# Performance work log

Hardware: AMD Instinct MI355X
Metric: run time of the kernel (lower is better)

## Reference

```python
import jax, jax.numpy as jnp
import numpy as np

N, T, DF, H, NH, E = 512, 60, 6, 64, 2, 8192
NEG = -1e10

def _leaky(x):
    return jnp.where(x >= 0, x, 0.01 * x)

def _ln(x, g, b, eps=1e-5):
    m = x.mean(-1, keepdims=True)
    v = ((x - m) ** 2).mean(-1, keepdims=True)
    return (x - m) / jnp.sqrt(v + eps) * g + b

def _gru_layer(xs, wih, whh, bih, bhh):
    # xs: (N, T, H_in) -> (N, T, H); torch GRU gate math
    h0 = jnp.zeros((xs.shape[0], whh.shape[1]), xs.dtype)
    def step(h, xt):
        gi = xt @ wih.T + bih
        gh = h @ whh.T + bhh
        ir, iz, inn = jnp.split(gi, 3, -1)
        hr, hz, hn = jnp.split(gh, 3, -1)
        r = jax.nn.sigmoid(ir + hr)
        z = jax.nn.sigmoid(iz + hz)
        n = jnp.tanh(inn + r * hn)
        h = (1 - z) * n + z * h
        return h, h
    _, hs = jax.lax.scan(step, h0, jnp.swapaxes(xs, 0, 1))
    return jnp.swapaxes(hs, 0, 1)

def _forward(x, edge_index, fc_in_w, fc_in_b, gru_wih0, gru_whh0, gru_bih0, gru_bhh0, gru_wih1, gru_whh1, gru_bih1, gru_bhh1, dm_qw, dm_kw, dm_vw, dm_vb, ssa_qw, ssa_kw, ssa_vw, ssa_vb, ln1_g, ln1_b, ln2_g, ln2_b, mlp_w1, mlp_b1, mlp_w2, mlp_b2, mha_in_w, mha_in_b, mha_out_w, mha_out_b, gf_xs_w, gf_xt_w, gf_xt_b, gf_h_w, gf_h_b, lin_w, lin_b):
    h = x @ fc_in_w.T + fc_in_b                      # (N, T, H)
    # temporal encoder: 2-layer GRU + leaky relu
    g = _gru_layer(h, gru_wih0, gru_whh0, gru_bih0, gru_bhh0)
    g = _gru_layer(g, gru_wih1, gru_whh1, gru_bih1, gru_bhh1)
    ts = _leaky(g)
    res_ts = ts[:, -1, :]                            # (N, H)
    # spatial sparse transformer: time T acts as batch, attention over stocks N
    xs = jnp.swapaxes(h, 0, 1)                       # (T, N, H)
    hd = H // NH
    q = (xs @ dm_qw.T).reshape(T, N, NH, hd).transpose(0, 2, 1, 3)
    k = (xs @ dm_kw.T).reshape(T, N, NH, hd).transpose(0, 2, 1, 3)
    v = (xs @ dm_vw.T + dm_vb).reshape(T, N, NH, hd).transpose(0, 2, 1, 3)
    attn = jnp.einsum('thnd,thmd->thnm', q, k) * (H ** -0.5)  # scale uses full dim C, as in source
    dmask = attn >= attn.mean(-1, keepdims=True)     # dynamic per-row mean threshold
    attn_s = jax.nn.softmax(jnp.where(dmask, attn, NEG), axis=-1)
    dyn = jnp.einsum('thnm,thmd->thnd', attn_s, v).transpose(0, 2, 1, 3).reshape(T, N, H)
    # SSA: static graph mask from edge_index
    qs = xs @ ssa_qw.T
    ks2 = xs @ ssa_kw.T
    vs = xs @ ssa_vw.T + ssa_vb
    a2 = jnp.einsum('tnc,tmc->tnm', qs, ks2) * (H ** -0.5)
    adj = jnp.zeros((N, N), jnp.float32).at[edge_index[0], edge_index[1]].add(1.0)
    gmask = adj >= 1.0
    a2s = jax.nn.softmax(jnp.where(gmask[None, :, :], a2, NEG), axis=-1)
    stat = jnp.einsum('tnm,tmc->tnc', a2s, vs)
    residual = dyn + stat + xs
    o = _ln(residual, ln1_g, ln1_b)
    o = (o @ mlp_w1.T + mlp_b1) @ mlp_w2.T + mlp_b2  # two linears, no activation (as in source)
    o = _ln(o + residual, ln2_g, ln2_b)
    move = _leaky(o)                                 # (T, N, H)
    # spatial embedding aggregation: sinusoidal PE + 1-head MHA over time
    pos = jnp.arange(T, dtype=jnp.float32)[:, None]
    div = jnp.exp(jnp.arange(0, H, 2, dtype=jnp.float32) * (-np.log(10000.0) / H))
    pe = jnp.zeros((T, H), jnp.float32).at[:, 0::2].set(jnp.sin(pos * div)).at[:, 1::2].set(jnp.cos(pos * div))
    src = move + pe[:, None, :]
    mq, mk, mv = jnp.split(src @ mha_in_w.T + mha_in_b, 3, axis=-1)
    sc = jnp.einsum('tnh,snh->nts', mq, mk) * (H ** -0.5)
    mo = jnp.einsum('nts,snh->tnh', jax.nn.softmax(sc, -1), mv) @ mha_out_w.T + mha_out_b
    agg = mo[-1]                                     # (N, H)
    mu = agg.mean(-1, keepdims=True)
    var = ((agg - mu) ** 2).mean(-1, keepdims=True)
    agg = (agg - mu) / jnp.sqrt(var + 1e-5)          # param-free layer_norm
    # gated fusion
    zg = jax.nn.sigmoid(agg @ gf_xs_w.T + res_ts @ gf_xt_w.T + gf_xt_b)
    fused = _leaky((zg * agg + (1 - zg) * res_ts) @ gf_h_w.T + gf_h_b)
    out = (fused @ lin_w.T + lin_b)[:, 0]
    return out, attn_s

def setup_inputs() -> dict:
    key = jax.random.key(0)
    ks = jax.random.split(key, 40)
    def w(i, shape):
        return jax.random.normal(ks[i], shape, jnp.float32) * 0.05
    return {
        'x': jax.random.normal(ks[0], (N, T, DF), jnp.float32),
        'edge_index': jax.random.randint(ks[1], (2, E), 0, N),
        'fc_in_w': w(2, (H, DF)), 'fc_in_b': w(3, (H,)),
        'gru_wih0': w(4, (3 * H, H)), 'gru_whh0': w(5, (3 * H, H)), 'gru_bih0': w(6, (3 * H,)), 'gru_bhh0': w(7, (3 * H,)),
        'gru_wih1': w(8, (3 * H, H)), 'gru_whh1': w(9, (3 * H, H)), 'gru_bih1': w(10, (3 * H,)), 'gru_bhh1': w(11, (3 * H,)),
        'dm_qw': w(12, (H, H)), 'dm_kw': w(13, (H, H)), 'dm_vw': w(14, (H, H)), 'dm_vb': w(15, (H,)),
        'ssa_qw': w(16, (H, H)), 'ssa_kw': w(17, (H, H)), 'ssa_vw': w(18, (H, H)), 'ssa_vb': w(19, (H,)),
        'ln1_g': jnp.ones((H,), jnp.float32), 'ln1_b': jnp.zeros((H,), jnp.float32),
        'ln2_g': jnp.ones((H,), jnp.float32), 'ln2_b': jnp.zeros((H,), jnp.float32),
        'mlp_w1': w(20, (2 * H, H)), 'mlp_b1': w(21, (2 * H,)), 'mlp_w2': w(22, (H, 2 * H)), 'mlp_b2': w(23, (H,)),
        'mha_in_w': w(24, (3 * H, H)), 'mha_in_b': w(25, (3 * H,)), 'mha_out_w': w(26, (H, H)), 'mha_out_b': w(27, (H,)),
        'gf_xs_w': w(28, (H, H)), 'gf_xt_w': w(29, (H, H)), 'gf_xt_b': w(30, (H,)),
        'gf_h_w': w(31, (H, H)), 'gf_h_b': w(32, (H,)),
        'lin_w': w(33, (1, H)), 'lin_b': w(34, (1,)),
    }

def reference(x, edge_index, fc_in_w, fc_in_b, gru_wih0, gru_whh0, gru_bih0, gru_bhh0, gru_wih1, gru_whh1, gru_bih1, gru_bhh1, dm_qw, dm_kw, dm_vw, dm_vb, ssa_qw, ssa_kw, ssa_vw, ssa_vb, ln1_g, ln1_b, ln2_g, ln2_b, mlp_w1, mlp_b1, mlp_w2, mlp_b2, mha_in_w, mha_in_b, mha_out_w, mha_out_b, gf_xs_w, gf_xt_w, gf_xt_b, gf_h_w, gf_h_b, lin_w, lin_b):
    return _forward(x, edge_index, fc_in_w, fc_in_b, gru_wih0, gru_whh0, gru_bih0, gru_bhh0, gru_wih1, gru_whh1, gru_bih1, gru_bhh1, dm_qw, dm_kw, dm_vw, dm_vb, ssa_qw, ssa_kw, ssa_vw, ssa_vb, ln1_g, ln1_b, ln2_g, ln2_b, mlp_w1, mlp_b1, mlp_w2, mlp_b2, mha_in_w, mha_in_b, mha_out_w, mha_out_b, gf_xs_w, gf_xt_w, gf_xt_b, gf_h_w, gf_h_b, lin_w, lin_b)
```

## Files before the change

kernel.cpp:

```cpp
#include <hip/hip_runtime.h>
#include <hip/hip_bf16.h>

#define NN 512
#define TT 60
#define DFF 6
#define EE 8192
#define TN (TT*NN)
#define TCH 20
#define NCHK 3
#define SCALEV 0.125f
#define NEGV -1.0e10f

typedef __hip_bfloat16 bf16;
using bfrag8 = __attribute__((ext_vector_type(8))) short;
using facc4  = __attribute__((ext_vector_type(4))) float;

__device__ __forceinline__ float b2f(bf16 v){ return __bfloat162float(v); }
__device__ __forceinline__ bf16 f2b(float v){ return __float2bfloat16(v); }
__device__ __forceinline__ float lk(float x){ return x >= 0.f ? x : 0.01f*x; }
__device__ __forceinline__ float sgm(float x){ return 1.f/(1.f+__expf(-x)); }

__device__ __forceinline__ float ldf(const float* p, long i){ return p[i]; }
__device__ __forceinline__ float ldf(const bf16* p, long i){ return b2f(p[i]); }
__device__ __forceinline__ void stf(float* p, long i, float v){ p[i] = v; }
__device__ __forceinline__ void stf(bf16* p, long i, float v){ p[i] = f2b(v); }

__device__ __forceinline__ float4 ld4f(const float* p){ return *(const float4*)p; }
__device__ __forceinline__ float4 ld4f(const bf16* p){
  ushort4 u = *(const ushort4*)p;
  float4 f;
  f.x = b2f(*(const bf16*)&u.x);
  f.y = b2f(*(const bf16*)&u.y);
  f.z = b2f(*(const bf16*)&u.z);
  f.w = b2f(*(const bf16*)&u.w);
  return f;
}

__device__ __forceinline__ float wsum64(float v){
  #pragma unroll
  for (int off = 32; off; off >>= 1) v += __shfl_xor(v, off, 64);
  return v;
}
__device__ __forceinline__ float wmax64(float v){
  #pragma unroll
  for (int off = 32; off; off >>= 1) v = fmaxf(v, __shfl_xor(v, off, 64));
  return v;
}

__global__ __launch_bounds__(256) void k_pack(
  const float* __restrict__ qw, const float* __restrict__ kw,
  const float* __restrict__ qsw, const float* __restrict__ ksw,
  const float* __restrict__ vw, const float* __restrict__ vsw,
  const float* __restrict__ vb, const float* __restrict__ vsb,
  const int* __restrict__ ei, unsigned int* __restrict__ msk,
  float* __restrict__ Wall, float* __restrict__ bcV)
{
  __shared__ unsigned int lmsk[8192];
  int tid = threadIdx.x;
  if (blockIdx.x == 97) {
    for (int i = tid; i < 8192; i += 256) lmsk[i] = 0u;
    __syncthreads();
    for (int e = tid; e < EE; e += 256) {
      int u = ei[e], v = ei[EE + e];
      atomicOr(&lmsk[u*16 + (v >> 5)], 1u << (v & 31));
    }
    __syncthreads();
    for (int i = tid; i < 8192; i += 256) msk[i] = lmsk[i];
    return;
  }
  int idx = blockIdx.x*256 + tid;
  if (idx < 6*4096) {
    int which = idx >> 12, rem = idx & 4095;
    const float* s = (which==0)?qw:(which==1)?kw:(which==2)?qsw:(which==3)?ksw:(which==4)?vw:vsw;
    Wall[idx] = s[rem];
  } else if (idx < 6*4096 + 128) {
    int o = idx - 6*4096;
    bcV[o] = (o < 64) ? vb[o] : vsb[o-64];
  }
}

__global__ __launch_bounds__(256) void k_fcin(
  const float* __restrict__ x, const float* __restrict__ w, const float* __restrict__ b,
  float* __restrict__ xs, float* __restrict__ resid)
{
  long idx = (long)blockIdx.x*256 + threadIdx.x;
  int o = idx & 63;
  long r = idx >> 6;
  int t = (int)(r / NN), n = (int)(r % NN);
  const float* xr = x + ((long)n*TT + t)*DFF;
  const float* wr = w + o*DFF;
  float acc = 0.f;
  #pragma unroll
  for (int j = 0; j < DFF; ++j) acc = fmaf(xr[j], wr[j], acc);
  float h = __fadd_rn(acc, b[o]);
  xs[idx] = h;
  resid[idx] = h;
}

__global__ __launch_bounds__(256) void k_proj(
  const float* __restrict__ A, const float* __restrict__ Wall, const float* __restrict__ bcV,
  float* __restrict__ qkx, float* __restrict__ qkc, bf16* __restrict__ vvc)
{
  __shared__ float As[64][68];
  __shared__ float Bs[64][68];
  int rt = blockIdx.x, bcn = blockIdx.y;
  const float* B = Wall + bcn*4096;
  int tid = threadIdx.x;
  int tx = tid & 15, ty = tid >> 4;
  float acc[4][4] = {{0.f}};
  #pragma unroll
  for (int i = 0; i < 4; ++i) {
    int t = i*256 + tid;
    int m = t >> 4, kq = (t & 15)*4;
    float4 av = *(const float4*)&A[(long)(rt*64 + m)*64 + kq];
    As[kq+0][m] = av.x; As[kq+1][m] = av.y; As[kq+2][m] = av.z; As[kq+3][m] = av.w;
    float4 bv = *(const float4*)&B[(long)m*64 + kq];
    Bs[kq+0][m] = bv.x; Bs[kq+1][m] = bv.y; Bs[kq+2][m] = bv.z; Bs[kq+3][m] = bv.w;
  }
  __syncthreads();
  for (int kk = 0; kk < 64; ++kk) {
    float4 a4 = *(const float4*)&As[kk][ty*4];
    float4 b4 = *(const float4*)&Bs[kk][tx*4];
    acc[0][0] = fmaf(a4.x,b4.x,acc[0][0]); acc[0][1] = fmaf(a4.x,b4.y,acc[0][1]); acc[0][2] = fmaf(a4.x,b4.z,acc[0][2]); acc[0][3] = fmaf(a4.x,b4.w,acc[0][3]);
    acc[1][0] = fmaf(a4.y,b4.x,acc[1][0]); acc[1][1] = fmaf(a4.y,b4.y,acc[1][1]); acc[1][2] = fmaf(a4.y,b4.z,acc[1][2]); acc[1][3] = fmaf(a4.y,b4.w,acc[1][3]);
    acc[2][0] = fmaf(a4.z,b4.x,acc[2][0]); acc[2][1] = fmaf(a4.z,b4.y,acc[2][1]); acc[2][2] = fmaf(a4.z,b4.z,acc[2][2]); acc[2][3] = fmaf(a4.z,b4.w,acc[2][3]);
    acc[3][0] = fmaf(a4.w,b4.x,acc[3][0]); acc[3][1] = fmaf(a4.w,b4.y,acc[3][1]); acc[3][2] = fmaf(a4.w,b4.z,acc[3][2]); acc[3][3] = fmaf(a4.w,b4.w,acc[3][3]);
  }
  if (bcn < 4) {
    float* C = (bcn < 2) ? qkx : qkc;
    int cb = (bcn & 1)*64;
    #pragma unroll
    for (int i = 0; i < 4; ++i) {
      long ro = (long)(rt*64 + ty*4 + i)*128 + cb + tx*4;
      #pragma unroll
      for (int j = 0; j < 4; ++j) C[ro + j] = acc[i][j];
    }
  } else {
    int cb = (bcn - 4)*64;
    float bv[4];
    #pragma unroll
    for (int j = 0; j < 4; ++j) bv[j] = bcV[cb + tx*4 + j];
    #pragma unroll
    for (int i = 0; i < 4; ++i) {
      long ro = (long)(rt*64 + ty*4 + i)*128 + cb + tx*4;
      #pragma unroll
      for (int j = 0; j < 4; ++j) vvc[ro + j] = f2b(acc[i][j] + bv[j]);
    }
  }
}

template<typename TA, typename TC>
__global__ __launch_bounds__(256) void k_gemm(
  const TA* __restrict__ A, const float* __restrict__ B, const float* __restrict__ bias,
  TC* __restrict__ C, int KD, int NC, int gather)
{
  __shared__ float As[64][68];
  __shared__ float Bs[64][68];
  int rt = blockIdx.x, bcn = blockIdx.y;
  int tid = threadIdx.x;
  int tx = tid & 15, ty = tid >> 4;
  float acc[4][4] = {{0.f}};
  int nch = KD >> 6;
  for (int kc = 0; kc < nch; ++kc) {
    __syncthreads();
    #pragma unroll
    for (int i = 0; i < 4; ++i) {
      int t = i*256 + tid;
      int m = t >> 4, kq = (t & 15)*4;
      long aoff;
      int r = rt*64 + m;
      if (gather) { int n2 = r / TT, t2 = r - n2*TT; aoff = ((long)t2*NN + n2)*64 + kc*64 + kq; }
      else aoff = (long)r*KD + kc*64 + kq;
      float4 av = ld4f(A + aoff);
      As[kq+0][m] = av.x; As[kq+1][m] = av.y; As[kq+2][m] = av.z; As[kq+3][m] = av.w;
      int col = bcn*64 + m;
      float4 bv = *(const float4*)&B[(long)col*KD + kc*64 + kq];
      Bs[kq+0][m] = bv.x; Bs[kq+1][m] = bv.y; Bs[kq+2][m] = bv.z; Bs[kq+3][m] = bv.w;
    }
    __syncthreads();
    #pragma unroll 8
    for (int kk = 0; kk < 64; ++kk) {
      float4 a4 = *(const float4*)&As[kk][ty*4];
      float4 b4 = *(const float4*)&Bs[kk][tx*4];
      acc[0][0] += a4.x*b4.x; acc[0][1] += a4.x*b4.y; acc[0][2] += a4.x*b4.z; acc[0][3] += a4.x*b4.w;
      acc[1][0] += a4.y*b4.x; acc[1][1] += a4.y*b4.y; acc[1][2] += a4.y*b4.z; acc[1][3] += a4.y*b4.w;
      acc[2][0] += a4.z*b4.x; acc[2][1] += a4.z*b4.y; acc[2][2] += a4.z*b4.z; acc[2][3] += a4.z*b4.w;
      acc[3][0] += a4.w*b4.x; acc[3][1] += a4.w*b4.y; acc[3][2] += a4.w*b4.z; acc[3][3] += a4.w*b4.w;
    }
  }
  float bv[4];
  #pragma unroll
  for (int j = 0; j < 4; ++j) bv[j] = bias ? bias[bcn*64 + tx*4 + j] : 0.f;
  #pragma unroll
  for (int i = 0; i < 4; ++i) {
    long ro = (long)(rt*64 + ty*4 + i)*NC + bcn*64 + tx*4;
    #pragma unroll
    for (int j = 0; j < 4; ++j) stf(C, ro + j, acc[i][j] + bv[j]);
  }
}

__global__ __launch_bounds__(192) void k_gru(
  const float* __restrict__ gi, const float* __restrict__ whh, const float* __restrict__ bhh,
  bf16* __restrict__ g_out, float* __restrict__ res_out, int layer)
{
  int n = blockIdx.x;
  int tid = threadIdx.x;
  int g = tid >> 6, o = tid & 63;
  __shared__ __align__(16) float h_lds[64];
  __shared__ float ghs[3][64];
  float4 w4[16];
  #pragma unroll
  for (int k4 = 0; k4 < 16; ++k4)
    w4[k4] = *(const float4*)&whh[(long)(g*64+o)*64 + k4*4];
  float bh = bhh[g*64+o];
  if (tid < 64) h_lds[tid] = 0.f;
  __syncthreads();
  const float4* h4 = (const float4*)h_lds;
  for (int t = 0; t < TT; ++t) {
    float p0 = 0.f, p1 = 0.f, p2 = 0.f, p3 = 0.f;
    #pragma unroll
    for (int k4 = 0; k4 < 16; ++k4) {
      float4 hv = h4[k4];
      p0 = fmaf(w4[k4].x, hv.x, p0);
      p1 = fmaf(w4[k4].y, hv.y, p1);
      p2 = fmaf(w4[k4].z, hv.z, p2);
      p3 = fmaf(w4[k4].w, hv.w, p3);
    }
    ghs[g][o] = bh + ((p0 + p1) + (p2 + p3));
    __syncthreads();
    if (tid < 64) {
      const float* gib = gi + ((long)n*TT + t)*192;
      float ir = gib[o], iz = gib[64+o], inn = gib[128+o];
      float r = sgm(ir + ghs[0][o]);
      float z = sgm(iz + ghs[1][o]);
      float nn2 = tanhf(inn + r*ghs[2][o]);
      float hn = (1.f - z)*nn2 + z*h_lds[o];
      h_lds[o] = hn;
      if (layer == 0) g_out[((long)t*NN + n)*64 + o] = f2b(hn);
      else if (t == TT-1) res_out[(long)n*64 + o] = lk(hn);
    }
    __syncthreads();
  }
}

#define MULADD4(QV, KV) \
  v0 = __fadd_rn(v0, __fmul_rn((QV).x, (KV).x)); \
  v1 = __fadd_rn(v1, __fmul_rn((QV).y, (KV).y)); \
  v2 = __fadd_rn(v2, __fmul_rn((QV).z, (KV).z)); \
  v3 = __fadd_rn(v3, __fmul_rn((QV).w, (KV).w));

__global__ __launch_bounds__(256, 3) void k_attn(
  const float* __restrict__ qkx, const float* __restrict__ qkc,
  const bf16* __restrict__ vvc, const unsigned int* __restrict__ msk,
  float* __restrict__ attn_out, float* __restrict__ resid, int tc)
{
  __shared__ __align__(16) char smem[52288];
  int qt = blockIdx.x, lt = blockIdx.z;
  int gt = tc*TCH + lt;
  int tid = threadIdx.x, tx = tid & 31, grp = tid >> 5;
  int qbase = grp*2;

  if (blockIdx.y == 2) {
    float* kc  = (float*)smem;
    bf16*  vTh = (bf16*)smem;
    float* qtl = (float*)(smem + 34816);
    bf16*  P   = (bf16*)(smem + 34816);

    float4* q4 = (float4*)qtl;
    float4* k4 = (float4*)kc;

    {
      int m = tid >> 4, jc = tid & 15;
      q4[m*17 + jc] = *(const float4*)(qkc + ((long)(lt*NN + qt*16 + m))*128 + jc*4);
    }

    float S[2][16];
    for (int p = 0; p < 4; ++p) {
      __syncthreads();
      for (int i = tid; i < 2048; i += 256) {
        int m = i >> 4, jc = i & 15;
        k4[m*17 + (jc ^ ((m >> 2) & 3))] =
          *(const float4*)(qkc + ((long)(lt*NN + p*128 + m))*128 + 64 + jc*4);
      }
      __syncthreads();
      float acc00 = 0.f, acc01 = 0.f, acc02 = 0.f, acc03 = 0.f;
      float acc10 = 0.f, acc11 = 0.f, acc12 = 0.f, acc13 = 0.f;
      #pragma unroll 4
      for (int jc = 0; jc < 16; ++jc) {
        float4 q0 = q4[(qbase+0)*17 + jc];
        float4 q1 = q4[(qbase+1)*17 + jc];
        float4 kv;
        int m0 = tx;
        kv = k4[m0*17 + (jc ^ ((m0 >> 2) & 3))];
        acc00 += q0.x*kv.x + q0.y*kv.y + q0.z*kv.z + q0.w*kv.w;
        acc10 += q1.x*kv.x + q1.y*kv.y + q1.z*kv.z + q1.w*kv.w;
        int m1 = tx + 32;
        kv = k4[m1*17 + (jc ^ ((m1 >> 2) & 3))];
        acc01 += q0.x*kv.x + q0.y*kv.y + q0.z*kv.z + q0.w*kv.w;
        acc11 += q1.x*kv.x + q1.y*kv.y + q1.z*kv.z + q1.w*kv.w;
        int m2 = tx + 64;
        kv = k4[m2*17 + (jc ^ ((m2 >> 2) & 3))];
        acc02 += q0.x*kv.x + q0.y*kv.y + q0.z*kv.z + q0.w*kv.w;
        acc12 += q1.x*kv.x + q1.y*kv.y + q1.z*kv.z + q1.w*kv.w;
        int m3 = tx + 96;
        kv = k4[m3*17 + (jc ^ ((m3 >> 2) & 3))];
        acc03 += q0.x*kv.x + q0.y*kv.y + q0.z*kv.z + q0.w*kv.w;
        acc13 += q1.x*kv.x + q1.y*kv.y + q1.z*kv.z + q1.w*kv.w;
      }
      S[0][p*4+0] = acc00; S[0][p*4+1] = acc01; S[0][p*4+2] = acc02; S[0][p*4+3] = acc03;
      S[1][p*4+0] = acc10; S[1][p*4+1] = acc11; S[1][p*4+2] = acc12; S[1][p*4+3] = acc13;
    }
    __syncthreads();

    #pragma unroll
    for (int qi = 0; qi < 2; ++qi) {
      #pragma unroll
      for (int ig = 0; ig < 16; ++ig) S[qi][ig] *= SCALEV;
      float lm = -INFINITY;
      #pragma unroll
      for (int ig = 0; ig < 16; ++ig) {
        bool keep = ((msk[(qt*16 + qbase + qi)*16 + ig] >> tx) & 1u) != 0u;
        float v = keep ? S[qi][ig] : NEGV;
        S[qi][ig] = v;
        lm = fmaxf(lm, v);
      }
      #pragma unroll
      for (int mk = 1; mk < 32; mk <<= 1) lm = fmaxf(lm, __shfl_xor(lm, mk, 64));
      float se = 0.f;
      #pragma unroll
      for (int ig = 0; ig < 16; ++ig) {
        float ev = __expf(S[qi][ig] - lm);
        S[qi][ig] = ev;
        se += ev;
      }
      #pragma unroll
      for (int mk = 1; mk < 32; mk <<= 1) se += __shfl_xor(se, mk, 64);
      float inv = 1.f / se;
      bf16* prow = P + (qbase + qi)*520;
      #pragma unroll
      for (int ig = 0; ig < 16; ++ig)
        prow[tx + 32*ig] = f2b(S[qi][ig]*inv);
    }

    int w = tid >> 6, l = tid & 63;
    int arow = l & 15, kgrp = l >> 4;
    facc4 acc = {0.f, 0.f, 0.f, 0.f};
    for (int kh = 0; kh < 2; ++kh) {
      __syncthreads();
      for (int i = tid; i < 2048; i += 256) {
        int m2 = (i & 127) << 1;
        int cc = (i >> 7) << 2;
        const bf16* gp = vvc + ((long)(lt*NN + kh*256 + m2))*128 + 64 + cc;
        ushort4 a = *(const ushort4*)(gp);
        ushort4 b = *(const ushort4*)(gp + 128);
        *(unsigned*)(vTh + (cc+0)*264 + m2) = (unsigned)a.x | ((unsigned)b.x << 16);
        *(unsigned*)(vTh + (cc+1)*264 + m2) = (unsigned)a.y | ((unsigned)b.y << 16);
        *(unsigned*)(vTh + (cc+2)*264 + m2) = (unsigned)a.z | ((unsigned)b.z << 16);
        *(unsigned*)(vTh + (cc+3)*264 + m2) = (unsigned)a.w | ((unsigned)b.w << 16);
      }
      __syncthreads();
      const bf16* pa = P + arow*520 + kh*256 + kgrp*8;
      const bf16* pb = vTh + (w*16 + arow)*264 + kgrp*8;
      #pragma unroll
      for (int ks = 0; ks < 8; ++ks) {
        bfrag8 av = *(const bfrag8*)(pa + ks*32);
        bfrag8 bv = *(const bfrag8*)(pb + ks*32);
        acc = __builtin_amdgcn_mfma_f32_16x16x32_bf16(av, bv, acc, 0, 0, 0);
      }
    }
    long rb = ((long)gt*NN + qt*16)*64 + w*16 + arow;
    #pragma unroll
    for (int r = 0; r < 4; ++r) {
      int row = kgrp*4 + r;
      resid[rb + (long)row*64] += acc[r];
    }
    return;
  }

  float* sc    = (float*)smem;
  bf16*  vT    = (bf16*)smem;
  float* kt    = (float*)(smem + 33280);
  bf16*  p_lds = (bf16*)(smem + 33280);
  float* red   = (float*)(smem + 49920);
  float* ulds  = (float*)(smem + 51712);
  float* means = (float*)(smem + 52224);

  int h = blockIdx.y;
  int qce = h*32, kce = 64 + h*32;

  float4 q0r[8], q1r[8];
  {
    const float* qp = qkx + ((long)(lt*NN + qt*16 + qbase))*128 + qce;
    #pragma unroll
    for (int j = 0; j < 8; ++j) q0r[j] = *(const float4*)(qp + j*4);
    #pragma unroll
    for (int j = 0; j < 8; ++j) q1r[j] = *(const float4*)(qp + 128 + j*4);
  }

  float S[2][16];
  for (int p = 0; p < 4; ++p) {
    __syncthreads();
    for (int i = tid; i < 1024; i += 256) {
      int row = i >> 3, jj = (i & 7) << 2;
      *(float4*)(kt + row*36 + jj) =
        *(const float4*)(qkx + ((long)(lt*NN + p*128 + row))*128 + kce + jj);
    }
    __syncthreads();
    #pragma unroll
    for (int ii = 0; ii < 4; ++ii) {
      int m = tx + 32*ii;
      const float4* kr4 = (const float4*)(kt + m*36);
      float4 k0 = kr4[0], k1 = kr4[1], k2 = kr4[2], k3 = kr4[3];
      float4 k4 = kr4[4], k5 = kr4[5], k6 = kr4[6], k7 = kr4[7];
      {
        float v0 = 0.f, v1 = 0.f, v2 = 0.f, v3 = 0.f;
        MULADD4(q0r[0], k0); MULADD4(q0r[1], k1); MULADD4(q0r[2], k2); MULADD4(q0r[3], k3);
        MULADD4(q0r[4], k4); MULADD4(q0r[5], k5); MULADD4(q0r[6], k6); MULADD4(q0r[7], k7);
        float s = __fadd_rn(__fadd_rn(v0, v1), __fadd_rn(v2, v3));
        s = s * 0.125f;
        S[0][p*4+ii] = s;
        sc[(qbase+0)*520 + p*128 + m] = s;
      }
      {
        float v0 = 0.f, v1 = 0.f, v2 = 0.f, v3 = 0.f;
        MULADD4(q1r[0], k0); MULADD4(q1r[1], k1); MULADD4(q1r[2], k2); MULADD4(q1r[3], k3);
        MULADD4(q1r[4], k4); MULADD4(q1r[5], k5); MULADD4(q1r[6], k6); MULADD4(q1r[7], k7);
        float s = __fadd_rn(__fadd_rn(v0, v1), __fadd_rn(v2, v3));
        s = s * 0.125f;
        S[1][p*4+ii] = s;
        sc[(qbase+1)*520 + p*128 + m] = s;
      }
    }
  }
  __syncthreads();
  if (tid < 128) {
    int row = tid >> 3, b = (tid >> 1) & 3, hh = tid & 1;
    const float* a = sc + row*520 + b*128 + hh*4;
    float4 r4 = *(const float4*)a;
    #pragma unroll
    for (int i = 8; i < 128; i += 8) {
      float4 v = *(const float4*)(a + i);
      r4.x = __fadd_rn(r4.x, v.x); r4.y = __fadd_rn(r4.y, v.y);
      r4.z = __fadd_rn(r4.z, v.z); r4.w = __fadd_rn(r4.w, v.w);
    }
    ulds[row*8 + b*2 + hh] = __fadd_rn(__fadd_rn(r4.x, r4.y), __fadd_rn(r4.z, r4.w));
  }
  __syncthreads();
  if (tid < 16) {
    const float* ur = ulds + tid*8;
    float p0 = __fadd_rn(ur[0], ur[1]);
    float p1 = __fadd_rn(ur[2], ur[3]);
    float p2 = __fadd_rn(ur[4], ur[5]);
    float p3 = __fadd_rn(ur[6], ur[7]);
    means[tid] = __fadd_rn(__fadd_rn(p0, p1), __fadd_rn(p2, p3)) * (1.f/512.f);
  }
  __syncthreads();

  long obase = ((long)(gt*2 + h))*NN*NN;
  #pragma unroll
  for (int qi = 0; qi < 2; ++qi) {
    float mn = means[qbase + qi];
    unsigned kmask = 0; float lm = -INFINITY;
    #pragma unroll
    for (int ig = 0; ig < 16; ++ig) {
      if (S[qi][ig] >= mn) { kmask |= (1u << ig); lm = fmaxf(lm, S[qi][ig]); }
    }
    #pragma unroll
    for (int mk = 1; mk < 32; mk <<= 1) lm = fmaxf(lm, __shfl_xor(lm, mk, 64));
    float e[16]; float se = 0.f;
    #pragma unroll
    for (int ig = 0; ig < 16; ++ig) {
      e[ig] = ((kmask >> ig) & 1u) ? __expf(S[qi][ig] - lm) : 0.f;
      se += e[ig];
    }
    #pragma unroll
    for (int mk = 1; mk < 32; mk <<= 1) se += __shfl_xor(se, mk, 64);
    float inv = 1.f/se;
    float* rowp = attn_out + obase + (long)(qt*16 + qbase + qi)*NN;
    bf16* prow = p_lds + (qbase + qi)*520;
    #pragma unroll
    for (int ig = 0; ig < 16; ++ig) {
      float pr = e[ig]*inv;
      rowp[tx + 32*ig] = pr;
      prow[tx + 32*ig] = f2b(pr);
    }
  }

  for (int i = tid; i < 2048; i += 256) {
    int m2 = (i & 255) << 1;
    int cc = (i >> 8) << 2;
    const bf16* gp = vvc + ((long)(lt*NN + m2))*128 + qce + cc;
    ushort4 a = *(const ushort4*)(gp);
    ushort4 b = *(const ushort4*)(gp + 128);
    *(unsigned*)(vT + (cc+0)*520 + m2) = (unsigned)a.x | ((unsigned)b.x << 16);
    *(unsigned*)(vT + (cc+1)*520 + m2) = (unsigned)a.y | ((unsigned)b.y << 16);
    *(unsigned*)(vT + (cc+2)*520 + m2) = (unsigned)a.z | ((unsigned)b.z << 16);
    *(unsigned*)(vT + (cc+3)*520 + m2) = (unsigned)a.w | ((unsigned)b.w << 16);
  }
  __syncthreads();

  {
    int w = tid >> 6, l = tid & 63;
    int nh = w & 1, kh = w >> 1;
    int arow = l & 15, kgrp = l >> 4;
    facc4 acc = {0.f, 0.f, 0.f, 0.f};
    const bf16* pa = p_lds + arow*520 + kh*256 + kgrp*8;
    const bf16* pb = vT + (nh*16 + arow)*520 + kh*256 + kgrp*8;
    #pragma unroll
    for (int ks = 0; ks < 8; ++ks) {
      bfrag8 av = *(const bfrag8*)(pa + ks*32);
      bfrag8 bv = *(const bfrag8*)(pb + ks*32);
      acc = __builtin_amdgcn_mfma_f32_16x16x32_bf16(av, bv, acc, 0, 0, 0);
    }
    if (w >= 2) {
      #pragma unroll
      for (int r = 0; r < 4; ++r)
        red[nh*272 + (kgrp*4 + r)*17 + arow] = acc[r];
    }
    __syncthreads();
    if (w < 2) {
      long rb = ((long)gt*NN + qt*16)*64 + h*32 + nh*16 + arow;
      #pragma unroll
      for (int r = 0; r < 4; ++r) {
        int row = kgrp*4 + r;
        resid[rb + (long)row*64] += acc[r] + red[nh*272 + row*17 + arow];
      }
    }
  }
}

__global__ __launch_bounds__(256) void k_mlp1(
  const float* __restrict__ resid, const float* __restrict__ g1, const float* __restrict__ b1,
  const float* __restrict__ B, const float* __restrict__ bias, float* __restrict__ C)
{
  __shared__ float As[64][68];
  __shared__ float Bs[64][68];
  int rt = blockIdx.x, bcn = blockIdx.y;
  int tid = threadIdx.x;
  int tx = tid & 15, ty = tid >> 4;
  int wave = tid >> 6, lane = tid & 63;
  for (int rr = wave; rr < 64; rr += 4) {
    float v = resid[((long)rt*64 + rr)*64 + lane];
    float m = wsum64(v)*(1.f/64.f);
    float d = v - m;
    float var = wsum64(d*d)*(1.f/64.f);
    As[lane][rr] = d*rsqrtf(var + 1e-5f)*g1[lane] + b1[lane];
  }
  #pragma unroll
  for (int i = 0; i < 4; ++i) {
    int t = i*256 + tid;
    int m = t >> 4, kq = (t & 15)*4;
    float4 bv = *(const float4*)&B[(long)(bcn*64 + m)*64 + kq];
    Bs[kq+0][m] = bv.x; Bs[kq+1][m] = bv.y; Bs[kq+2][m] = bv.z; Bs[kq+3][m] = bv.w;
  }
  __syncthreads();
  float acc[4][4] = {{0.f}};
  #pragma unroll 8
  for (int kk = 0; kk < 64; ++kk) {
    float4 a4 = *(const float4*)&As[kk][ty*4];
    float4 b4 = *(const float4*)&Bs[kk][tx*4];
    acc[0][0] += a4.x*b4.x; acc[0][1] += a4.x*b4.y; acc[0][2] += a4.x*b4.z; acc[0][3] += a4.x*b4.w;
    acc[1][0] += a4.y*b4.x; acc[1][1] += a4.y*b4.y; acc[1][2] += a4.y*b4.z; acc[1][3] += a4.y*b4.w;
    acc[2][0] += a4.z*b4.x; acc[2][1] += a4.z*b4.y; acc[2][2] += a4.z*b4.z; acc[2][3] += a4.z*b4.w;
    acc[3][0] += a4.w*b4.x; acc[3][1] += a4.w*b4.y; acc[3][2] += a4.w*b4.z; acc[3][3] += a4.w*b4.w;
  }
  #pragma unroll
  for (int i = 0; i < 4; ++i) {
    long ro = (long)(rt*64 + ty*4 + i)*128 + bcn*64 + tx*4;
    #pragma unroll
    for (int j = 0; j < 4; ++j) C[ro + j] = acc[i][j] + bias[bcn*64 + tx*4 + j];
  }
}

__global__ __launch_bounds__(256) void k_mha_in(
  const float* __restrict__ mlpo, const float* __restrict__ resid,
  const float* __restrict__ g2, const float* __restrict__ b2,
  const float* __restrict__ B, const float* __restrict__ bias, bf16* __restrict__ C)
{
  __shared__ float As[64][68];
  __shared__ float Bs[64][68];
  int rt = blockIdx.x, bcn = blockIdx.y;
  int tid = threadIdx.x;
  int tx = tid & 15, ty = tid >> 4;
  int wave = tid >> 6, lane = tid & 63;
  for (int rr = wave; rr < 64; rr += 4) {
    long r = (long)rt*64 + rr;
    float v = mlpo[r*64 + lane] + resid[r*64 + lane];
    float m = wsum64(v)*(1.f/64.f);
    float d = v - m;
    float var = wsum64(d*d)*(1.f/64.f);
    float y = d*rsqrtf(var + 1e-5f)*g2[lane] + b2[lane];
    y = lk(y);
    float tf = (float)(r / NN);
    float dv = __expf(-(float)(lane & ~1) * 0.14391156831212787f);
    float pe = (lane & 1) ? cosf(tf*dv) : sinf(tf*dv);
    As[lane][rr] = y + pe;
  }
  #pragma unroll
  for (int i = 0; i < 4; ++i) {
    int t = i*256 + tid;
    int m = t >> 4, kq = (t & 15)*4;
    float4 bv = *(const float4*)&B[(long)(bcn*64 + m)*64 + kq];
    Bs[kq+0][m] = bv.x; Bs[kq+1][m] = bv.y; Bs[kq+2][m] = bv.z; Bs[kq+3][m] = bv.w;
  }
  __syncthreads();
  float acc[4][4] = {{0.f}};
  #pragma unroll 8
  for (int kk = 0; kk < 64; ++kk) {
    float4 a4 = *(const float4*)&As[kk][ty*4];
    float4 b4 = *(const float4*)&Bs[kk][tx*4];
    acc[0][0] += a4.x*b4.x; acc[0][1] += a4.x*b4.y; acc[0][2] += a4.x*b4.z; acc[0][3] += a4.x*b4.w;
    acc[1][0] += a4.y*b4.x; acc[1][1] += a4.y*b4.y; acc[1][2] += a4.y*b4.z; acc[1][3] += a4.y*b4.w;
    acc[2][0] += a4.z*b4.x; acc[2][1] += a4.z*b4.y; acc[2][2] += a4.z*b4.z; acc[2][3] += a4.z*b4.w;
    acc[3][0] += a4.w*b4.x; acc[3][1] += a4.w*b4.y; acc[3][2] += a4.w*b4.z; acc[3][3] += a4.w*b4.w;
  }
  #pragma unroll
  for (int i = 0; i < 4; ++i) {
    long ro = (long)(rt*64 + ty*4 + i)*192 + bcn*64 + tx*4;
    #pragma unroll
    for (int j = 0; j < 4; ++j) C[ro + j] = f2b(acc[i][j] + bias[bcn*64 + tx*4 + j]);
  }
}

__global__ __launch_bounds__(64) void k_head(
  const bf16* __restrict__ mqkv, const float* __restrict__ rts,
  const float* __restrict__ mow, const float* __restrict__ mob,
  const float* __restrict__ xsw, const float* __restrict__ xtw, const float* __restrict__ xtb,
  const float* __restrict__ hw, const float* __restrict__ hb,
  const float* __restrict__ linw, const float* __restrict__ linb,
  float* __restrict__ out)
{
  int n = blockIdx.x, o = threadIdx.x;
  __shared__ float ps[TT];
  __shared__ float buf[64], buf2[64];
  float mq = b2f(mqkv[((long)(TT-1)*NN + n)*192 + o]);
  for (int s = 0; s < TT; ++s) {
    float v = mq * b2f(mqkv[((long)s*NN + n)*192 + 64 + o]);
    v = wsum64(v);
    if (o == 0) ps[s] = v * SCALEV;
  }
  __syncthreads();
  float x = (o < TT) ? ps[o] : -INFINITY;
  float mx = wmax64(x);
  float e = (o < TT) ? __expf(x - mx) : 0.f;
  float se = wsum64(e);
  if (o < TT) ps[o] = e / se;
  __syncthreads();
  float acc = 0.f;
  for (int s = 0; s < TT; ++s) acc += ps[s]*b2f(mqkv[((long)s*NN + n)*192 + 128 + o]);
  buf[o] = acc;
  __syncthreads();
  float acc2 = mob[o];
  for (int k = 0; k < 64; ++k) acc2 += buf[k]*mow[o*64 + k];
  float m2 = wsum64(acc2)*(1.f/64.f);
  float d2 = acc2 - m2;
  float var2 = wsum64(d2*d2)*(1.f/64.f);
  float a = d2*rsqrtf(var2 + 1e-5f);
  float rt = rts[(long)n*64 + o];
  __syncthreads();
  buf[o] = a; buf2[o] = rt;
  __syncthreads();
  float pre = xtb[o];
  for (int k = 0; k < 64; ++k) pre += buf[k]*xsw[o*64 + k] + buf2[k]*xtw[o*64 + k];
  float zg = sgm(pre);
  float u = zg*a + (1.f - zg)*rt;
  __syncthreads();
  buf[o] = u;
  __syncthreads();
  float f = hb[o];
  for (int k = 0; k < 64; ++k) f += buf[k]*hw[o*64 + k];
  f = lk(f);
  float tot = wsum64(f * linw[o]);
  if (o == 0) out[n] = tot + linb[0];
}

extern "C" void kernel_launch(void* const* d_in, const int* in_sizes, int n_in,
                              void* d_out, int out_size, void* d_ws, size_t ws_size,
                              hipStream_t stream)
{
  const float* x    = (const float*)d_in[0];
  const int*   ei   = (const int*)  d_in[1];
  const float* fcw  = (const float*)d_in[2];
  const float* fcb  = (const float*)d_in[3];
  const float* wih0 = (const float*)d_in[4];
  const float* whh0 = (const float*)d_in[5];
  const float* bih0 = (const float*)d_in[6];
  const float* bhh0 = (const float*)d_in[7];
  const float* wih1 = (const float*)d_in[8];
  const float* whh1 = (const float*)d_in[9];
  const float* bih1 = (const float*)d_in[10];
  const float* bhh1 = (const float*)d_in[11];
  const float* dmqw = (const float*)d_in[12];
  const float* dmkw = (const float*)d_in[13];
  const float* dmvw = (const float*)d_in[14];
  const float* dmvb = (const float*)d_in[15];
  const float* ssqw = (const float*)d_in[16];
  const float* sskw = (const float*)d_in[17];
  const float* ssvw = (const float*)d_in[18];
  const float* ssvb = (const float*)d_in[19];
  const float* ln1g = (const float*)d_in[20];
  const float* ln1b = (const float*)d_in[21];
  const float* ln2g = (const float*)d_in[22];
  const float* ln2b = (const float*)d_in[23];
  const float* mw1  = (const float*)d_in[24];
  const float* mb1  = (const float*)d_in[25];
  const float* mw2  = (const float*)d_in[26];
  const float* mb2  = (const float*)d_in[27];
  const float* mhw  = (const float*)d_in[28];
  const float* mhb  = (const float*)d_in[29];
  const float* mow  = (const float*)d_in[30];
  const float* mob  = (const float*)d_in[31];
  const float* gxsw = (const float*)d_in[32];
  const float* gxtw = (const float*)d_in[33];
  const float* gxtb = (const float*)d_in[34];
  const float* ghw  = (const float*)d_in[35];
  const float* ghb  = (const float*)d_in[36];
  const float* linw = (const float*)d_in[37];
  const float* linb = (const float*)d_in[38];

  char* base = (char*)d_ws;
  float*  xs    = (float*)(base);
  char*   Rb    = base + 7864320;
  float*  qkc   = (float*)Rb;
  bf16*   vvc   = (bf16*)(Rb + 5242880);
  float*  qkx   = (float*)(Rb + 7864320);
  float*  mlph  = (float*)Rb;
  bf16*   mqkv  = (bf16*)Rb;
  bf16*   g0    = (bf16*)(base + 23592960);
  float*  resid = (float*)(base + 27525120);
  float*  rts   = (float*)(base + 43253760);
  unsigned int* msk = (unsigned int*)(base + 43384832);
  float*  Wall  = (float*)(base + 43417600);
  float*  bcV   = (float*)(base + 43515904);
  float*  mlpo  = xs;
  float*  outb  = (float*)d_out;
  float*  attn  = outb + 512;
  float*  gi    = (float*)((char*)d_out + 2048);

  k_pack<<<dim3(98), 256, 0, stream>>>(dmqw, dmkw, ssqw, sskw, dmvw, ssvw, dmvb, ssvb, ei, msk, Wall, bcV);
  k_fcin<<<dim3(TN*64/256), 256, 0, stream>>>(x, fcw, fcb, xs, resid);
  k_gemm<float,float><<<dim3(480, 3), 256, 0, stream>>>(xs, wih0, bih0, gi, 64, 192, 1);
  k_gru<<<dim3(NN), 192, 0, stream>>>(gi, whh0, bhh0, g0, nullptr, 0);
  k_gemm<bf16,float><<<dim3(480, 3), 256, 0, stream>>>(g0, wih1, bih1, gi, 64, 192, 1);
  k_gru<<<dim3(NN), 192, 0, stream>>>(gi, whh1, bhh1, nullptr, rts, 1);
  for (int tc = 0; tc < NCHK; ++tc) {
    const float* xsc = xs + (size_t)tc*TCH*NN*64;
    k_proj<<<dim3(TCH*NN/64, 6), 256, 0, stream>>>(xsc, Wall, bcV, qkx, qkc, vvc);
    k_attn<<<dim3(32, 3, TCH), 256, 0, stream>>>(qkx, qkc, vvc, msk, attn, resid, tc);
  }
  k_mlp1<<<dim3(480, 2), 256, 0, stream>>>(resid, ln1g, ln1b, mw1, mb1, mlph);
  k_gemm<float,float><<<dim3(480, 1), 256, 0, stream>>>(mlph, mw2, mb2, mlpo, 128, 64, 0);
  k_mha_in<<<dim3(480, 3), 256, 0, stream>>>(mlpo, resid, ln2g, ln2b, mhw, mhb, mqkv);
  k_head<<<dim3(NN), 64, 0, stream>>>(mqkv, rts, mow, mob, gxsw, gxtw, gxtb, ghw, ghb, linw, linb, outb);
}
```

Baseline: 732.3 us.

## Prefetch GRU inputs, remap attention blocks, split SSA residual, nontemporal attn stores

The GRU kernel now loads the next timestep's input gates during the current step, which takes the global-load latency off the serial recurrence. The attention launch becomes a 1D grid with a swizzled block mapping that spreads related blocks across XCDs. The SSA branch writes its contribution to a separate resid2 buffer instead of doing a read-modify-write on resid, and the downstream MLP and MHA kernels add the two buffers. The large attention probability output is written with nontemporal stores to reduce cache pollution. In exchange this needs an extra workspace buffer and extra reads in the later kernels.

```diff
diff --git a/kernel.cpp b/kernel.cpp
--- a/kernel.cpp
+++ b/kernel.cpp
@@ -213,7 +213,12 @@
   for (int k4 = 0; k4 < 16; ++k4)
     w4[k4] = *(const float4*)&whh[(long)(g*64+o)*64 + k4*4];
   float bh = bhh[g*64+o];
-  if (tid < 64) h_lds[tid] = 0.f;
+  float ir = 0.f, iz = 0.f, inn = 0.f;
+  if (tid < 64) {
+    h_lds[tid] = 0.f;
+    const float* gp = gi + ((long)n*TT + 0)*192;
+    ir = gp[o]; iz = gp[64+o]; inn = gp[128+o];
+  }
   __syncthreads();
   const float4* h4 = (const float4*)h_lds;
   for (int t = 0; t < TT; ++t) {
@@ -229,8 +234,6 @@
     ghs[g][o] = bh + ((p0 + p1) + (p2 + p3));
     __syncthreads();
     if (tid < 64) {
-      const float* gib = gi + ((long)n*TT + t)*192;
-      float ir = gib[o], iz = gib[64+o], inn = gib[128+o];
       float r = sgm(ir + ghs[0][o]);
       float z = sgm(iz + ghs[1][o]);
       float nn2 = tanhf(inn + r*ghs[2][o]);
@@ -238,6 +241,10 @@
       h_lds[o] = hn;
       if (layer == 0) g_out[((long)t*NN + n)*64 + o] = f2b(hn);
       else if (t == TT-1) res_out[(long)n*64 + o] = lk(hn);
+      if (t + 1 < TT) {
+        const float* gp = gi + ((long)n*TT + t + 1)*192;
+        ir = gp[o]; iz = gp[64+o]; inn = gp[128+o];
+      }
     }
     __syncthreads();
   }
@@ -252,15 +259,21 @@
 __global__ __launch_bounds__(256, 3) void k_attn(
   const float* __restrict__ qkx, const float* __restrict__ qkc,
   const bf16* __restrict__ vvc, const unsigned int* __restrict__ msk,
-  float* __restrict__ attn_out, float* __restrict__ resid, int tc)
+  float* __restrict__ attn_out, float* __restrict__ resid,
+  float* __restrict__ resid2, int tc)
 {
   __shared__ __align__(16) char smem[52288];
-  int qt = blockIdx.x, lt = blockIdx.z;
+  int bid = blockIdx.x;
+  int vid = (bid & 7)*240 + (bid >> 3);
+  int lt = vid / 96;
+  int rem = vid - lt*96;
+  int yy = rem >> 5;
+  int qt = rem & 31;
   int gt = tc*TCH + lt;
   int tid = threadIdx.x, tx = tid & 31, grp = tid >> 5;
   int qbase = grp*2;
 
-  if (blockIdx.y == 2) {
+  if (yy == 2) {
     float* kc  = (float*)smem;
     bf16*  vTh = (bf16*)smem;
     float* qtl = (float*)(smem + 34816);
@@ -372,7 +385,7 @@
     #pragma unroll
     for (int r = 0; r < 4; ++r) {
       int row = kgrp*4 + r;
-      resid[rb + (long)row*64] += acc[r];
+      resid2[rb + (long)row*64] = acc[r];
     }
     return;
   }
@@ -385,7 +398,7 @@
   float* ulds  = (float*)(smem + 51712);
   float* means = (float*)(smem + 52224);
 
-  int h = blockIdx.y;
+  int h = yy;
   int qce = h*32, kce = 64 + h*32;
 
   float4 q0r[8], q1r[8];
@@ -481,7 +494,7 @@
     #pragma unroll
     for (int ig = 0; ig < 16; ++ig) {
       float pr = e[ig]*inv;
-      rowp[tx + 32*ig] = pr;
+      __builtin_nontemporal_store(pr, rowp + tx + 32*ig);
       prow[tx + 32*ig] = f2b(pr);
     }
   }
@@ -530,7 +543,8 @@
 }
 
 __global__ __launch_bounds__(256) void k_mlp1(
-  const float* __restrict__ resid, const float* __restrict__ g1, const float* __restrict__ b1,
+  const float* __restrict__ resid, const float* __restrict__ resid2,
+  const float* __restrict__ g1, const float* __restrict__ b1,
   const float* __restrict__ B, const float* __restrict__ bias, float* __restrict__ C)
 {
   __shared__ float As[64][68];
@@ -540,7 +554,8 @@
   int tx = tid & 15, ty = tid >> 4;
   int wave = tid >> 6, lane = tid & 63;
   for (int rr = wave; rr < 64; rr += 4) {
-    float v = resid[((long)rt*64 + rr)*64 + lane];
+    long idx = ((long)rt*64 + rr)*64 + lane;
+    float v = resid[idx] + resid2[idx];
     float m = wsum64(v)*(1.f/64.f);
     float d = v - m;
     float var = wsum64(d*d)*(1.f/64.f);
@@ -574,6 +589,7 @@
 
 __global__ __launch_bounds__(256) void k_mha_in(
   const float* __restrict__ mlpo, const float* __restrict__ resid,
+  const float* __restrict__ resid2,
   const float* __restrict__ g2, const float* __restrict__ b2,
   const float* __restrict__ B, const float* __restrict__ bias, bf16* __restrict__ C)
 {
@@ -585,7 +601,8 @@
   int wave = tid >> 6, lane = tid & 63;
   for (int rr = wave; rr < 64; rr += 4) {
     long r = (long)rt*64 + rr;
-    float v = mlpo[r*64 + lane] + resid[r*64 + lane];
+    float rf = resid[r*64 + lane] + resid2[r*64 + lane];
+    float v = mlpo[r*64 + lane] + rf;
     float m = wsum64(v)*(1.f/64.f);
     float d = v - m;
     float var = wsum64(d*d)*(1.f/64.f);
@@ -728,6 +745,7 @@
   bf16*   mqkv  = (bf16*)Rb;
   bf16*   g0    = (bf16*)(base + 23592960);
   float*  resid = (float*)(base + 27525120);
+  float*  resid2= (float*)(base + 35389440);
   float*  rts   = (float*)(base + 43253760);
   unsigned int* msk = (unsigned int*)(base + 43384832);
   float*  Wall  = (float*)(base + 43417600);
@@ -746,10 +764,10 @@
   for (int tc = 0; tc < NCHK; ++tc) {
     const float* xsc = xs + (size_t)tc*TCH*NN*64;
     k_proj<<<dim3(TCH*NN/64, 6), 256, 0, stream>>>(xsc, Wall, bcV, qkx, qkc, vvc);
-    k_attn<<<dim3(32, 3, TCH), 256, 0, stream>>>(qkx, qkc, vvc, msk, attn, resid, tc);
-  }
-  k_mlp1<<<dim3(480, 2), 256, 0, stream>>>(resid, ln1g, ln1b, mw1, mb1, mlph);
+    k_attn<<<dim3(1920), 256, 0, stream>>>(qkx, qkc, vvc, msk, attn, resid, resid2, tc);
+  }
+  k_mlp1<<<dim3(480, 2), 256, 0, stream>>>(resid, resid2, ln1g, ln1b, mw1, mb1, mlph);
   k_gemm<float,float><<<dim3(480, 1), 256, 0, stream>>>(mlph, mw2, mb2, mlpo, 128, 64, 0);
-  k_mha_in<<<dim3(480, 3), 256, 0, stream>>>(mlpo, resid, ln2g, ln2b, mhw, mhb, mqkv);
+  k_mha_in<<<dim3(480, 3), 256, 0, stream>>>(mlpo, resid, resid2, ln2g, ln2b, mhw, mhb, mqkv);
   k_head<<<dim3(NN), 64, 0, stream>>>(mqkv, rts, mow, mob, gxsw, gxtw, gxtb, ghw, ghb, linw, linb, outb);
 }
```

Result: no change. 735.2 us (+0.4%).
